# Kernel optimization log

Measured on AMD Instinct MI355X. Metric: run time of the kernel, lower is better.

The kernel has to match this reference:

```python
import jax, jax.numpy as jnp
import numpy as np

TOP_K = 2  # cfg.MODEL.MOE.TOP_K


def setup_inputs() -> dict:
    key = jax.random.key(0)
    ks = jax.random.split(key, 5)
    bs, L, d_in, d_out, E = 32, 1024, 768, 256, 8
    return {
        "x": jax.random.normal(ks[0], (bs, L, d_in), dtype=jnp.float32),
        "gate_W": jax.random.normal(ks[1], (d_in, E), dtype=jnp.float32) * (1.0 / np.sqrt(d_in)),
        "gate_b": jax.random.normal(ks[2], (E,), dtype=jnp.float32) * 0.01,
        "expert_W": jax.random.normal(ks[3], (E, d_in, d_out), dtype=jnp.float32) * (1.0 / np.sqrt(d_in)),
        "expert_b": jax.random.normal(ks[4], (E, d_out), dtype=jnp.float32) * 0.01,
    }


def reference(x, gate_W, gate_b, expert_W, expert_b):
    # Gate: (bs, L, E) softmax over experts, then top-k routing weights.
    gate_logits = jnp.einsum("bli,ie->ble", x, gate_W) + gate_b
    gate_weights = jax.nn.softmax(gate_logits, axis=-1)
    topk_vals, topk_idx = jax.lax.top_k(gate_weights, TOP_K)  # (bs, L, K)

    # Dense all-expert projection (E is small), then gather the selected ones.
    # all_out: (bs, L, E, d_out)
    all_out = jnp.einsum("bli,eio->bleo", x, expert_W) + expert_b

    # Select top-k expert outputs per token: (bs, L, K, d_out)
    sel = jnp.take_along_axis(all_out, topk_idx[..., None], axis=2)

    # Weighted combine over the K routed experts -> (bs, L, d_out)
    output = jnp.sum(sel * topk_vals[..., None], axis=2)
    return output
```

## Files before the change

### kernel.cpp

```cpp
#include <hip/hip_runtime.h>
#include <hip/hip_bf16.h>
#include <stdint.h>

#define T_TOKENS 32768
#define D_IN     768
#define D_OUT    256
#define N_EXP    8
#define S_TOT    (T_TOKENS*2)
#define S_PAD    66560
#define KSPLIT   6
#define NKB      24

typedef __attribute__((ext_vector_type(8))) short bf16x8;
typedef __attribute__((ext_vector_type(4))) float f32x4;

__device__ __forceinline__ unsigned short f2bf(float f) {
    unsigned u = __float_as_uint(f);
    return (unsigned short)((u + 0x7FFFu + ((u >> 16) & 1u)) >> 16);
}
__device__ __forceinline__ unsigned pack_bf2(float a, float b) {
    return (unsigned)f2bf(a) | ((unsigned)f2bf(b) << 16);
}

__device__ __forceinline__ void async16(void* lds, const void* g) {
    __builtin_amdgcn_global_load_lds(
        (const __attribute__((address_space(1))) unsigned int*)g,
        (__attribute__((address_space(3))) unsigned int*)lds, 16, 0, 0);
}

__global__ __launch_bounds__(256) void convw_kernel(
        const float* __restrict__ W, unsigned short* __restrict__ WTb,
        int* __restrict__ zero16) {
    if (blockIdx.x == 0 && threadIdx.x < 16) zero16[threadIdx.x] = 0;
    int eb_ = blockIdx.x;
    int n = threadIdx.x;
    const float* src = W + ((size_t)(eb_ / NKB) * D_IN + (eb_ % NKB) * 32) * 256 + n;
    unsigned pk[16];
    #pragma unroll
    for (int j = 0; j < 16; j++)
        pk[j] = pack_bf2(src[(2*j) * 256], src[(2*j+1) * 256]);
    unsigned* dst = (unsigned*)(WTb + ((size_t)eb_ * 256 + n) * 32);
    #pragma unroll
    for (int j = 0; j < 16; j++) dst[j] = pk[j];
}

__global__ __launch_bounds__(64) void gate_partial_kernel(
        const float* __restrict__ x, const float* __restrict__ gW,
        unsigned short* __restrict__ xbf, float* __restrict__ partial) {
    __shared__ float tile[64 * 65];
    int tid = threadIdx.x;
    int t0  = blockIdx.x * 64;
    int kq  = blockIdx.y;
    int c16 = tid & 15, rb = tid >> 4;
    float acc[8] = {0,0,0,0,0,0,0,0};
    #pragma unroll 1
    for (int j = 0; j < 2; j++) {
        int kc = kq * 128 + j * 64;
        #pragma unroll
        for (int i = 0; i < 16; i++) {
            int row = i * 4 + rb;
            size_t g = (size_t)(t0 + row) * D_IN + kc + c16 * 4;
            float4 v = *(const float4*)(x + g);
            uint2 p; p.x = pack_bf2(v.x, v.y); p.y = pack_bf2(v.z, v.w);
            *(uint2*)(xbf + g) = p;
            float* d = &tile[row * 65 + c16 * 4];
            d[0] = v.x; d[1] = v.y; d[2] = v.z; d[3] = v.w;
        }
        __syncthreads();
        const float* gr = gW + (size_t)kc * 8;
        #pragma unroll 8
        for (int kk = 0; kk < 64; kk++) {
            float xv = tile[tid * 65 + kk];
            #pragma unroll
            for (int e = 0; e < 8; e++) acc[e] += xv * gr[kk * 8 + e];
        }
        __syncthreads();
    }
    float* dst = partial + ((size_t)kq * T_TOKENS + t0 + tid) * 8;
    float4 o0 = {acc[0], acc[1], acc[2], acc[3]};
    float4 o1 = {acc[4], acc[5], acc[6], acc[7]};
    *(float4*)dst = o0; *(float4*)(dst + 4) = o1;
}

__global__ __launch_bounds__(256) void gate_final_kernel(
        const float* __restrict__ partial, const float* __restrict__ gb,
        float* __restrict__ topk_w, int* __restrict__ topk_e, int* __restrict__ counts) {
    __shared__ int h[8];
    int tid = threadIdx.x;
    if (tid < 8) h[tid] = 0;
    __syncthreads();
    int t = blockIdx.x * 256 + tid;
    float acc[8] = {0,0,0,0,0,0,0,0};
    #pragma unroll
    for (int q = 0; q < KSPLIT; q++) {
        const float* p = partial + ((size_t)q * T_TOKENS + t) * 8;
        float4 a = *(const float4*)p;
        float4 b = *(const float4*)(p + 4);
        acc[0] += a.x; acc[1] += a.y; acc[2] += a.z; acc[3] += a.w;
        acc[4] += b.x; acc[5] += b.y; acc[6] += b.z; acc[7] += b.w;
    }
    float mx = -1e30f;
    #pragma unroll
    for (int e = 0; e < 8; e++) { acc[e] += gb[e]; mx = fmaxf(mx, acc[e]); }
    float w[8], s = 0.f;
    #pragma unroll
    for (int e = 0; e < 8; e++) { w[e] = expf(acc[e] - mx); s += w[e]; }
    float inv = 1.0f / s;
    int e0 = 0; float b0 = -1.f;
    #pragma unroll
    for (int e = 0; e < 8; e++) if (w[e] > b0) { b0 = w[e]; e0 = e; }
    int e1 = 0; float b1 = -1.f;
    #pragma unroll
    for (int e = 0; e < 8; e++) if (e != e0 && w[e] > b1) { b1 = w[e]; e1 = e; }
    topk_w[t*2]   = b0 * inv;
    topk_w[t*2+1] = b1 * inv;
    topk_e[t*2]   = e0;
    topk_e[t*2+1] = e1;
    atomicAdd(&h[e0], 1); atomicAdd(&h[e1], 1);
    __syncthreads();
    if (tid < 8) atomicAdd(&counts[tid], h[tid]);
}

__global__ void scatter_kernel(const int* __restrict__ topk_e, const float* __restrict__ topk_w,
                               const int* __restrict__ counts, int* __restrict__ cursors,
                               int* __restrict__ slot_token, float* __restrict__ slot_w,
                               int* __restrict__ inv_slot) {
    int offs[9]; offs[0] = 0;
    #pragma unroll
    for (int e = 0; e < 8; e++) offs[e+1] = offs[e] + ((counts[e] + 127) & ~127);
    if (blockIdx.x == 0) {
        #pragma unroll
        for (int e = 0; e < 8; e++) {
            int start = offs[e] + counts[e];
            for (int i = start + threadIdx.x; i < offs[e+1]; i += 256) slot_w[i] = 0.f;
        }
    }
    __shared__ int hcnt[8], hbase[8];
    if (threadIdx.x < 8) hcnt[threadIdx.x] = 0;
    __syncthreads();
    int idx[4], ee[4], lr[4];
    int base = blockIdx.x * 256 * 4 + threadIdx.x;
    #pragma unroll
    for (int j = 0; j < 4; j++) {
        idx[j] = base + j * 256;
        ee[j]  = topk_e[idx[j]];
        lr[j]  = atomicAdd(&hcnt[ee[j]], 1);
    }
    __syncthreads();
    if (threadIdx.x < 8) hbase[threadIdx.x] = atomicAdd(&cursors[threadIdx.x], hcnt[threadIdx.x]);
    __syncthreads();
    #pragma unroll
    for (int j = 0; j < 4; j++) {
        int slot = offs[ee[j]] + hbase[ee[j]] + lr[j];
        slot_token[slot] = idx[j] >> 1;
        slot_w[slot]     = topk_w[idx[j]];
        inv_slot[idx[j]] = slot;
    }
}

template<bool ROUTED>
__global__ __launch_bounds__(512, 4) void moe_gemm_kernel(
        const unsigned short* __restrict__ xbf, const unsigned short* __restrict__ WTb,
        const float* __restrict__ eb, const int* __restrict__ counts,
        const int* __restrict__ slot_token, const float* __restrict__ slot_w,
        float* __restrict__ dst) {
    __shared__ unsigned short A_lds[3][128 * 32];

    int lbid = (blockIdx.x & 7) * ((int)gridDim.x >> 3) + (blockIdx.x >> 3);

    int offs[9]; offs[0] = 0;
    #pragma unroll
    for (int e = 0; e < 8; e++) offs[e+1] = offs[e] + ((counts[e] + 127) & ~127);
    int row0 = lbid * 128;
    if (row0 >= offs[8]) return;
    int expert = 0;
    #pragma unroll
    for (int e = 0; e < 8; e++) if (row0 >= offs[e]) expert = e;

    int tid  = threadIdx.x;
    int wave = tid >> 6, lane = tid & 63;
    int lrow = lane & 15, lquad = lane >> 4;
    int wm = wave >> 2, wn = wave & 3;

    int ar = tid >> 2, ap = tid & 3;
    int alc = (ap - (ar >> 1)) & 3;
    int tok = slot_token[row0 + ar];
    tok = (tok < 0 || tok >= T_TOKENS) ? 0 : tok;
    const unsigned short* asrc = xbf + (size_t)tok * D_IN + alc * 8;

    const unsigned short* bptr = WTb + (size_t)expert * NKB * 8192
                                     + (wn * 64 + lrow) * 32 + lquad * 8;

    int a_off[4];
    #pragma unroll
    for (int m = 0; m < 4; m++) {
        int r = wm * 64 + m * 16 + lrow;
        a_off[m] = r * 32 + ((lquad + (r >> 1)) & 3) * 8;
    }

    f32x4 acc[4][4];
    #pragma unroll
    for (int m = 0; m < 4; m++)
        #pragma unroll
        for (int q = 0; q < 4; q++) acc[m][q] = (f32x4){0,0,0,0};

    bf16x8 bA[4], bB[4];
    auto bload = [&](int kb, bf16x8 (&b)[4]) {
        const unsigned short* bp = bptr + (size_t)kb * 8192;
        #pragma unroll
        for (int q = 0; q < 4; q++) b[q] = *(const bf16x8*)(bp + q * 512);
    };

    auto kstep = [&](int s, bf16x8 (&bcur)[4], bf16x8 (&bnxt)[4]) {
        if (s == NKB - 1) asm volatile("s_waitcnt vmcnt(0)" ::: "memory");
        else              asm volatile("s_waitcnt vmcnt(5)" ::: "memory");
        asm volatile("s_barrier" ::: "memory");
        if (s + 1 < NKB) bload(s + 1, bnxt);
        if (s + 2 < NKB)
            async16(&A_lds[(s + 2) % 3][tid * 8], asrc + (s + 2) * 32);
        int p = s % 3;
        bf16x8 a[4];
        #pragma unroll
        for (int m = 0; m < 4; m++) a[m] = *(const bf16x8*)&A_lds[p][a_off[m]];
        __builtin_amdgcn_s_setprio(1);
        #pragma unroll
        for (int q = 0; q < 4; q++)
            #pragma unroll
            for (int m = 0; m < 4; m++)
                acc[m][q] = __builtin_amdgcn_mfma_f32_16x16x32_bf16(a[m], bcur[q], acc[m][q], 0, 0, 0);
        __builtin_amdgcn_s_setprio(0);
    };

    async16(&A_lds[0][tid * 8], asrc);
    __builtin_amdgcn_sched_barrier(0);
    bload(0, bA);
    async16(&A_lds[1][tid * 8], asrc + 32);
    for (int s = 0; s < NKB; s += 2) {
        kstep(s, bA, bB);
        kstep(s + 1, bB, bA);
    }

    float bias_q[4];
    #pragma unroll
    for (int q = 0; q < 4; q++)
        bias_q[q] = eb[expert * D_OUT + wn * 64 + q * 16 + lrow];
    #pragma unroll
    for (int m = 0; m < 4; m++) {
        #pragma unroll
        for (int r = 0; r < 4; r++) {
            int slot = row0 + wm * 64 + m * 16 + lquad * 4 + r;
            if constexpr (ROUTED) {
                float* drow = dst + (size_t)slot * D_OUT + wn * 64;
                #pragma unroll
                for (int q = 0; q < 4; q++)
                    drow[q * 16 + lrow] = acc[m][q][r] + bias_q[q];
            } else {
                int tk = slot_token[slot];
                float wgt = slot_w[slot];
                if (wgt != 0.f) {
                    #pragma unroll
                    for (int q = 0; q < 4; q++)
                        atomicAdd(dst + (size_t)tk * D_OUT + wn * 64 + q * 16 + lrow,
                                  wgt * (acc[m][q][r] + bias_q[q]));
                }
            }
        }
    }
}

__global__ void combine_kernel(const float* __restrict__ routed, const int* __restrict__ inv_slot,
                               const float* __restrict__ topk_w, float* __restrict__ out) {
    int flat = blockIdx.x * 256 + threadIdx.x;
    int t = flat >> 6, c = (flat & 63) * 4;
    int   s0 = inv_slot[t*2], s1 = inv_slot[t*2+1];
    float w0 = topk_w[t*2],   w1 = topk_w[t*2+1];
    float4 r0 = *(const float4*)(routed + (size_t)s0 * D_OUT + c);
    float4 r1 = *(const float4*)(routed + (size_t)s1 * D_OUT + c);
    float4 o;
    o.x = w0*r0.x + w1*r1.x; o.y = w0*r0.y + w1*r1.y;
    o.z = w0*r0.z + w1*r1.z; o.w = w0*r0.w + w1*r1.w;
    *(float4*)(out + (size_t)t * D_OUT + c) = o;
}

extern "C" void kernel_launch(void* const* d_in, const int* in_sizes, int n_in,
                              void* d_out, int out_size, void* d_ws, size_t ws_size,
                              hipStream_t stream) {
    const float* x  = (const float*)d_in[0];
    const float* gW = (const float*)d_in[1];
    const float* gb = (const float*)d_in[2];
    const float* eW = (const float*)d_in[3];
    const float* eb = (const float*)d_in[4];
    float* out = (float*)d_out;
    char* ws = (char*)d_ws;

    float* topk_w      = (float*)(ws + 0);
    int*   topk_e      = (int*)  (ws + 262144);
    int*   counts      = (int*)  (ws + 524288);
    int*   cursors     = (int*)  (ws + 524320);
    int*   slot_token  = (int*)  (ws + 524416);
    float* slot_w      = (float*)(ws + 790656);
    int*   inv_slot    = (int*)  (ws + 1056896);
    float* partial     = (float*)(ws + 1319040);
    unsigned short* WTb= (unsigned short*)(ws + 7610496);
    unsigned short* xbf= (unsigned short*)(ws + 10756224);
    float* routed      = (float*)(ws + 61087872);
    const size_t NEED_ROUTED = 61087872 + (size_t)S_PAD * D_OUT * 4;
    bool use_routed = (ws_size >= NEED_ROUTED);

    convw_kernel       <<<N_EXP * NKB, 256, 0, stream>>>(eW, WTb, counts);
    gate_partial_kernel<<<dim3(T_TOKENS / 64, KSPLIT), 64, 0, stream>>>(x, gW, xbf, partial);
    gate_final_kernel  <<<T_TOKENS / 256, 256, 0, stream>>>(partial, gb, topk_w, topk_e, counts);
    scatter_kernel     <<<S_TOT / (256 * 4), 256, 0, stream>>>(topk_e, topk_w, counts, cursors,
                                                               slot_token, slot_w, inv_slot);
    if (use_routed) {
        moe_gemm_kernel<true><<<S_PAD / 128, 512, 0, stream>>>(xbf, WTb, eb, counts,
                                                               slot_token, slot_w, routed);
        combine_kernel<<<T_TOKENS * D_OUT / 4 / 256, 256, 0, stream>>>(routed, inv_slot,
                                                                       topk_w, out);
    } else {
        hipMemsetAsync(slot_token, 0, 532480, stream);
        hipMemsetAsync(out, 0, (size_t)out_size * sizeof(float), stream);
        moe_gemm_kernel<false><<<S_PAD / 128, 512, 0, stream>>>(xbf, WTb, eb, counts,
                                                                slot_token, slot_w, out);
    }
}
```

Measured before the change: 262.0 us.

## Fuse gate partial-sum and top-k kernels into one block-per-32-tokens kernel

Merges the split-K gate matmul kernel and the gate finalize kernel into one kernel. Each 256-thread block handles 32 tokens across the full input dimension, staging gate weights in LDS and reducing partial sums across 8 lanes with shuffles before softmax and top-2. This removes the partial-sum buffer round trip through global memory and one kernel launch. In exchange each block does more serial work over K, and there are fewer, larger blocks.

```diff
diff --git a/kernel.cpp b/kernel.cpp
--- a/kernel.cpp
+++ b/kernel.cpp
@@ -8,7 +8,6 @@
 #define N_EXP    8
 #define S_TOT    (T_TOKENS*2)
 #define S_PAD    66560
-#define KSPLIT   6
 #define NKB      24
 
 typedef __attribute__((ext_vector_type(8))) short bf16x8;
@@ -44,81 +43,73 @@
     for (int j = 0; j < 16; j++) dst[j] = pk[j];
 }
 
-__global__ __launch_bounds__(64) void gate_partial_kernel(
+__global__ __launch_bounds__(256) void gate_fused_kernel(
         const float* __restrict__ x, const float* __restrict__ gW,
-        unsigned short* __restrict__ xbf, float* __restrict__ partial) {
-    __shared__ float tile[64 * 65];
+        const float* __restrict__ gb, unsigned short* __restrict__ xbf,
+        float* __restrict__ topk_w, int* __restrict__ topk_e,
+        int* __restrict__ counts) {
+    __shared__ float tile[32 * 133];
+    __shared__ float gws[1024];
+    __shared__ int h8[8];
     int tid = threadIdx.x;
-    int t0  = blockIdx.x * 64;
-    int kq  = blockIdx.y;
-    int c16 = tid & 15, rb = tid >> 4;
+    if (tid < 8) h8[tid] = 0;
+    int t0 = blockIdx.x * 32;
+    int kf = tid & 31, rb = tid >> 5;
+    int tt = tid >> 3, qq = tid & 7;
     float acc[8] = {0,0,0,0,0,0,0,0};
     #pragma unroll 1
-    for (int j = 0; j < 2; j++) {
-        int kc = kq * 128 + j * 64;
-        #pragma unroll
-        for (int i = 0; i < 16; i++) {
-            int row = i * 4 + rb;
-            size_t g = (size_t)(t0 + row) * D_IN + kc + c16 * 4;
+    for (int ch = 0; ch < 6; ++ch) {
+        int kc = ch * 128;
+        __syncthreads();
+        *(float4*)&gws[tid * 4] = *(const float4*)(gW + kc * 8 + tid * 4);
+        #pragma unroll
+        for (int i = 0; i < 4; ++i) {
+            int row = i * 8 + rb;
+            size_t g = (size_t)(t0 + row) * D_IN + kc + kf * 4;
             float4 v = *(const float4*)(x + g);
             uint2 p; p.x = pack_bf2(v.x, v.y); p.y = pack_bf2(v.z, v.w);
             *(uint2*)(xbf + g) = p;
-            float* d = &tile[row * 65 + c16 * 4];
+            float* d = &tile[row * 133 + kf * 4];
             d[0] = v.x; d[1] = v.y; d[2] = v.z; d[3] = v.w;
         }
         __syncthreads();
-        const float* gr = gW + (size_t)kc * 8;
-        #pragma unroll 8
-        for (int kk = 0; kk < 64; kk++) {
-            float xv = tile[tid * 65 + kk];
+        #pragma unroll
+        for (int kk = 0; kk < 16; ++kk) {
+            float xv = tile[tt * 133 + qq + 8 * kk];
+            const float* gp = &gws[(qq + 8 * kk) * 8];
             #pragma unroll
-            for (int e = 0; e < 8; e++) acc[e] += xv * gr[kk * 8 + e];
+            for (int e = 0; e < 8; ++e) acc[e] += xv * gp[e];
         }
-        __syncthreads();
-    }
-    float* dst = partial + ((size_t)kq * T_TOKENS + t0 + tid) * 8;
-    float4 o0 = {acc[0], acc[1], acc[2], acc[3]};
-    float4 o1 = {acc[4], acc[5], acc[6], acc[7]};
-    *(float4*)dst = o0; *(float4*)(dst + 4) = o1;
-}
-
-__global__ __launch_bounds__(256) void gate_final_kernel(
-        const float* __restrict__ partial, const float* __restrict__ gb,
-        float* __restrict__ topk_w, int* __restrict__ topk_e, int* __restrict__ counts) {
-    __shared__ int h[8];
-    int tid = threadIdx.x;
-    if (tid < 8) h[tid] = 0;
+    }
+    #pragma unroll
+    for (int e = 0; e < 8; ++e) {
+        acc[e] += __shfl_xor(acc[e], 1);
+        acc[e] += __shfl_xor(acc[e], 2);
+        acc[e] += __shfl_xor(acc[e], 4);
+    }
+    if (qq == 0) {
+        int t = t0 + tt;
+        float mx = -1e30f;
+        #pragma unroll
+        for (int e = 0; e < 8; ++e) { acc[e] += gb[e]; mx = fmaxf(mx, acc[e]); }
+        float w[8], s = 0.f;
+        #pragma unroll
+        for (int e = 0; e < 8; ++e) { w[e] = expf(acc[e] - mx); s += w[e]; }
+        float inv = 1.0f / s;
+        int e0 = 0; float b0 = -1.f;
+        #pragma unroll
+        for (int e = 0; e < 8; ++e) if (w[e] > b0) { b0 = w[e]; e0 = e; }
+        int e1 = 0; float b1 = -1.f;
+        #pragma unroll
+        for (int e = 0; e < 8; ++e) if (e != e0 && w[e] > b1) { b1 = w[e]; e1 = e; }
+        topk_w[t*2]   = b0 * inv;
+        topk_w[t*2+1] = b1 * inv;
+        topk_e[t*2]   = e0;
+        topk_e[t*2+1] = e1;
+        atomicAdd(&h8[e0], 1); atomicAdd(&h8[e1], 1);
+    }
     __syncthreads();
-    int t = blockIdx.x * 256 + tid;
-    float acc[8] = {0,0,0,0,0,0,0,0};
-    #pragma unroll
-    for (int q = 0; q < KSPLIT; q++) {
-        const float* p = partial + ((size_t)q * T_TOKENS + t) * 8;
-        float4 a = *(const float4*)p;
-        float4 b = *(const float4*)(p + 4);
-        acc[0] += a.x; acc[1] += a.y; acc[2] += a.z; acc[3] += a.w;
-        acc[4] += b.x; acc[5] += b.y; acc[6] += b.z; acc[7] += b.w;
-    }
-    float mx = -1e30f;
-    #pragma unroll
-    for (int e = 0; e < 8; e++) { acc[e] += gb[e]; mx = fmaxf(mx, acc[e]); }
-    float w[8], s = 0.f;
-    #pragma unroll
-    for (int e = 0; e < 8; e++) { w[e] = expf(acc[e] - mx); s += w[e]; }
-    float inv = 1.0f / s;
-    int e0 = 0; float b0 = -1.f;
-    #pragma unroll
-    for (int e = 0; e < 8; e++) if (w[e] > b0) { b0 = w[e]; e0 = e; }
-    int e1 = 0; float b1 = -1.f;
-    #pragma unroll
-    for (int e = 0; e < 8; e++) if (e != e0 && w[e] > b1) { b1 = w[e]; e1 = e; }
-    topk_w[t*2]   = b0 * inv;
-    topk_w[t*2+1] = b1 * inv;
-    topk_e[t*2]   = e0;
-    topk_e[t*2+1] = e1;
-    atomicAdd(&h[e0], 1); atomicAdd(&h[e1], 1);
-    __syncthreads();
-    if (tid < 8) atomicAdd(&counts[tid], h[tid]);
+    if (tid < 8) atomicAdd(&counts[tid], h8[tid]);
 }
 
 __global__ void scatter_kernel(const int* __restrict__ topk_e, const float* __restrict__ topk_w,
@@ -300,18 +291,17 @@
     int*   slot_token  = (int*)  (ws + 524416);
     float* slot_w      = (float*)(ws + 790656);
     int*   inv_slot    = (int*)  (ws + 1056896);
-    float* partial     = (float*)(ws + 1319040);
     unsigned short* WTb= (unsigned short*)(ws + 7610496);
     unsigned short* xbf= (unsigned short*)(ws + 10756224);
     float* routed      = (float*)(ws + 61087872);
     const size_t NEED_ROUTED = 61087872 + (size_t)S_PAD * D_OUT * 4;
     bool use_routed = (ws_size >= NEED_ROUTED);
 
-    convw_kernel       <<<N_EXP * NKB, 256, 0, stream>>>(eW, WTb, counts);
-    gate_partial_kernel<<<dim3(T_TOKENS / 64, KSPLIT), 64, 0, stream>>>(x, gW, xbf, partial);
-    gate_final_kernel  <<<T_TOKENS / 256, 256, 0, stream>>>(partial, gb, topk_w, topk_e, counts);
-    scatter_kernel     <<<S_TOT / (256 * 4), 256, 0, stream>>>(topk_e, topk_w, counts, cursors,
-                                                               slot_token, slot_w, inv_slot);
+    convw_kernel      <<<N_EXP * NKB, 256, 0, stream>>>(eW, WTb, counts);
+    gate_fused_kernel <<<T_TOKENS / 32, 256, 0, stream>>>(x, gW, gb, xbf,
+                                                          topk_w, topk_e, counts);
+    scatter_kernel    <<<S_TOT / (256 * 4), 256, 0, stream>>>(topk_e, topk_w, counts, cursors,
+                                                              slot_token, slot_w, inv_slot);
     if (use_routed) {
         moe_gemm_kernel<true><<<S_PAD / 128, 512, 0, stream>>>(xbf, WTb, eb, counts,
                                                                slot_token, slot_w, routed);
```

Result: faster. 255.5 us (-2.5%).
